# Optimization experiments

Measured on AMD Instinct MI355X. Metric: run time of the kernel, lower is better.

The kernel has to match this reference:

```python
import jax, jax.numpy as jnp
import numpy as np
import math

D_MODEL = 1024
HEADS = 16
HEAD_DIM = D_MODEL // HEADS
D_FF = 4096
EPS = 1e-5


def setup_inputs() -> dict:
    key = jax.random.key(0)
    ks = jax.random.split(key, 16)
    B, S, D = 4, 4096, D_MODEL
    s = 0.02
    return {
        "x": jax.random.normal(ks[0], (B, S, D), jnp.float32),
        "uncertainty": jax.random.uniform(ks[1], (HEADS,), jnp.float32),
        "Wq": jax.random.normal(ks[2], (D, D), jnp.float32) * s,
        "Wk": jax.random.normal(ks[3], (D, D), jnp.float32) * s,
        "Wv": jax.random.normal(ks[4], (D, D), jnp.float32) * s,
        "Wo": jax.random.normal(ks[5], (D, D), jnp.float32) * s,
        "bo": jnp.zeros((D,), jnp.float32),
        "ln1_g": jnp.ones((D,), jnp.float32),
        "ln1_b": jnp.zeros((D,), jnp.float32),
        "ln2_g": jnp.ones((D,), jnp.float32),
        "ln2_b": jnp.zeros((D,), jnp.float32),
        "W1": jax.random.normal(ks[6], (D, D_FF), jnp.float32) * s,
        "b1": jnp.zeros((D_FF,), jnp.float32),
        "W2": jax.random.normal(ks[7], (D_FF, D), jnp.float32) * s,
        "b2": jnp.zeros((D,), jnp.float32),
    }


def _layernorm(x, g, b):
    mu = jnp.mean(x, axis=-1, keepdims=True)
    var = jnp.mean(jnp.square(x - mu), axis=-1, keepdims=True)
    return (x - mu) * jax.lax.rsqrt(var + EPS) * g + b


def _attention(tmp, uncertainty, Wq, Wk, Wv, Wo, bo):
    B, S, D = tmp.shape
    # faithful to source: split_heads -> (B, S, head_dim, heads) via transpose(-2,-1)
    def split(y):
        return y.reshape(B, S, HEADS, HEAD_DIM).swapaxes(-2, -1)
    q = split(tmp @ Wq)  # (B,S,hd,H)
    k = split(tmp @ Wk)
    v = split(tmp @ Wv)
    scale = math.sqrt(HEAD_DIM) * jnp.sum(uncertainty)
    # per-token (head_dim x head_dim) scores, contracting over heads axis
    scores = jnp.einsum('bsih,bsjh->bsij', q, k) / scale  # (B,S,hd,hd)
    probs = jax.nn.softmax(scores, axis=-1)
    out = jnp.einsum('bsij,bsjh->bsih', probs, v)  # (B,S,hd,H)
    out = out.swapaxes(-2, -1).reshape(B, S, D)
    return out @ Wo + bo


def reference(x, uncertainty, Wq, Wk, Wv, Wo, bo, ln1_g, ln1_b, ln2_g, ln2_b, W1, b1, W2, b2):
    tmp = _layernorm(x, ln1_g, ln1_b)
    x = x + _attention(tmp, uncertainty, Wq, Wk, Wv, Wo, bo)  # dropout = identity (eval)
    tmp = _layernorm(x, ln2_g, ln2_b)
    ff = (jax.nn.gelu(tmp @ W1 + b1, approximate=False)) @ W2 + b2
    return x + ff
```

## Files before the change

kernel.cpp:

```cpp
#include <hip/hip_runtime.h>

typedef unsigned short u16;
typedef __attribute__((ext_vector_type(8))) short short8;
typedef __attribute__((ext_vector_type(4))) float f32x4;

static __device__ __forceinline__ float bf2f(u16 u) {
    union { unsigned int u; float f; } c; c.u = ((unsigned int)u) << 16; return c.f;
}
static __device__ __forceinline__ u16 f2bf(float f) {
    union { float f; unsigned int u; } c; c.f = f;
    unsigned int r = (c.u + 0x7fffu + ((c.u >> 16) & 1u)) >> 16;
    return (u16)r;
}

static __device__ __forceinline__ void glds16(const u16* g, u16* l) {
    __builtin_amdgcn_global_load_lds((const __attribute__((address_space(1))) unsigned int*)g,
                                     (__attribute__((address_space(3))) unsigned int*)l,
                                     16, 0, 0);
}

__global__ void wtrans_all(const float* __restrict__ q, const float* __restrict__ k,
                           const float* __restrict__ v, const float* __restrict__ o,
                           const float* __restrict__ w1, const float* __restrict__ w2,
                           u16* __restrict__ tqkv, u16* __restrict__ to_,
                           u16* __restrict__ t1, u16* __restrict__ t2) {
    const int id = blockIdx.x;
    const float* W; u16* D; int K, N, local;
    if (id < 3072) {
        const int which = id >> 10; local = id & 1023;
        W = which == 0 ? q : (which == 1 ? k : v);
        D = tqkv + (size_t)which * 1024 * 1024; K = 1024; N = 1024;
    } else if (id < 4096) { W = o;  D = to_; K = 1024; N = 1024; local = id - 3072; }
    else if (id < 8192)   { W = w1; D = t1;  K = 1024; N = 4096; local = id - 4096; }
    else                  { W = w2; D = t2;  K = 4096; N = 1024; local = id - 8192; }
    const int nx = N / 32;
    const int n0 = (local % nx) * 32, k0 = (local / nx) * 32;
    __shared__ float t[32][33];
    for (int i = threadIdx.y; i < 32; i += 8)
        t[i][threadIdx.x] = W[(size_t)(k0 + i) * N + n0 + threadIdx.x];
    __syncthreads();
    for (int i = threadIdx.y; i < 32; i += 8)
        D[(size_t)(n0 + i) * K + k0 + threadIdx.x] = f2bf(t[threadIdx.x][i]);
}

template <typename TI>
__global__ __launch_bounds__(256) void ln_kernel(const TI* __restrict__ x,
                                                 const float* __restrict__ g,
                                                 const float* __restrict__ b,
                                                 u16* __restrict__ out) {
    const int row = blockIdx.x;
    float4 v;
    if constexpr (sizeof(TI) == 4) {
        v = ((const float4*)((const float*)x + (size_t)row * 1024))[threadIdx.x];
    } else {
        ushort4 u = ((const ushort4*)((const u16*)x + (size_t)row * 1024))[threadIdx.x];
        v = make_float4(bf2f(u.x), bf2f(u.y), bf2f(u.z), bf2f(u.w));
    }
    float s = v.x + v.y + v.z + v.w;
    float ss = v.x * v.x + v.y * v.y + v.z * v.z + v.w * v.w;
    #pragma unroll
    for (int o = 32; o; o >>= 1) { s += __shfl_down(s, o); ss += __shfl_down(ss, o); }
    __shared__ float red[8];
    const int lane = threadIdx.x & 63, wave = threadIdx.x >> 6;
    if (lane == 0) { red[wave] = s; red[4 + wave] = ss; }
    __syncthreads();
    float S = red[0] + red[1] + red[2] + red[3];
    float SS = red[4] + red[5] + red[6] + red[7];
    float mu = S * (1.0f / 1024.0f);
    float var = SS * (1.0f / 1024.0f) - mu * mu;
    float rs = rsqrtf(var + 1e-5f);
    float4 gv = ((const float4*)g)[threadIdx.x];
    float4 bv = ((const float4*)b)[threadIdx.x];
    ushort4 o4;
    o4.x = f2bf((v.x - mu) * rs * gv.x + bv.x);
    o4.y = f2bf((v.y - mu) * rs * gv.y + bv.y);
    o4.z = f2bf((v.z - mu) * rs * gv.z + bv.z);
    o4.w = f2bf((v.w - mu) * rs * gv.w + bv.w);
    ((ushort4*)(out + (size_t)row * 1024))[threadIdx.x] = o4;
}

__global__ __launch_bounds__(256) void attn_kernel(const u16* __restrict__ QKV,
                                                   const float* __restrict__ unc,
                                                   u16* __restrict__ out) {
    __shared__ float kb[4][1024];
    __shared__ float vb[4][1024];
    const int tid = threadIdx.x;
    const int wave = tid >> 6, lane = tid & 63;
    const int tok = blockIdx.x * 4 + wave;
    const size_t baseq = (size_t)tok * 3072;

    #pragma unroll
    for (int e2 = 0; e2 < 2; e2++) {
        const int c = lane + 64 * e2;
        const int h = c >> 3, j0 = (c & 7) * 8;
        uint4 kraw = *(const uint4*)(QKV + baseq + 1024 + c * 8);
        uint4 vraw = *(const uint4*)(QKV + baseq + 2048 + c * 8);
        u16 kt[8], vt[8];
        *(uint4*)kt = kraw; *(uint4*)vt = vraw;
        #pragma unroll
        for (int e = 0; e < 8; e++) {
            kb[wave][(j0 + e) * 16 + h] = bf2f(kt[e]);
            vb[wave][(j0 + e) * 16 + h] = bf2f(vt[e]);
        }
    }
    float q[16];
    #pragma unroll
    for (int h = 0; h < 16; h++) q[h] = bf2f(QKV[baseq + h * 64 + lane]);
    float su = 0.0f;
    #pragma unroll
    for (int h = 0; h < 16; h++) su += unc[h];
    const float sinv = 1.0f / (8.0f * su);
    __syncthreads();

    float s[64];
    #pragma unroll
    for (int j = 0; j < 64; j++) {
        const float4* kr = (const float4*)&kb[wave][j * 16];
        float4 k0 = kr[0], k1 = kr[1], k2 = kr[2], k3 = kr[3];
        float a = q[0] * k0.x + q[1] * k0.y + q[2] * k0.z + q[3] * k0.w;
        a += q[4] * k1.x + q[5] * k1.y + q[6] * k1.z + q[7] * k1.w;
        a += q[8] * k2.x + q[9] * k2.y + q[10] * k2.z + q[11] * k2.w;
        a += q[12] * k3.x + q[13] * k3.y + q[14] * k3.z + q[15] * k3.w;
        s[j] = a;
    }
    float m = s[0];
    #pragma unroll
    for (int j = 1; j < 64; j++) m = fmaxf(m, s[j]);
    float sum = 0.0f;
    #pragma unroll
    for (int j = 0; j < 64; j++) { s[j] = __expf((s[j] - m) * sinv); sum += s[j]; }
    const float r = 1.0f / sum;
    float o[16];
    #pragma unroll
    for (int h = 0; h < 16; h++) o[h] = 0.0f;
    #pragma unroll
    for (int j = 0; j < 64; j++) {
        const float p = s[j];
        const float4* vr = (const float4*)&vb[wave][j * 16];
        float4 v0 = vr[0], v1 = vr[1], v2 = vr[2], v3 = vr[3];
        o[0] += p * v0.x; o[1] += p * v0.y; o[2] += p * v0.z; o[3] += p * v0.w;
        o[4] += p * v1.x; o[5] += p * v1.y; o[6] += p * v1.z; o[7] += p * v1.w;
        o[8] += p * v2.x; o[9] += p * v2.y; o[10] += p * v2.z; o[11] += p * v2.w;
        o[12] += p * v3.x; o[13] += p * v3.y; o[14] += p * v3.z; o[15] += p * v3.w;
    }
    const size_t baso = (size_t)tok * 1024;
    #pragma unroll
    for (int h = 0; h < 16; h++) out[baso + h * 64 + lane] = f2bf(o[h] * r);
}

template <int EPI>
__global__ __launch_bounds__(256, 2)
void gemm_kernel(const u16* __restrict__ A, const u16* __restrict__ Bt,
                 const float* __restrict__ bias, const void* __restrict__ res,
                 float* __restrict__ outF, u16* __restrict__ outB,
                 int N, int K) {
    __shared__ __align__(16) u16 As[128 * 64];
    __shared__ __align__(16) u16 Bs[128 * 64];
    const int tid = threadIdx.x;
    const int lane = tid & 63;
    const int wave = tid >> 6;
    const int wm = (wave >> 1) * 64;
    const int wn = (wave & 1) * 64;
    const int m0 = blockIdx.x * 128;
    const int n0 = blockIdx.y * 128;

    f32x4 acc[4][4];
    #pragma unroll
    for (int i = 0; i < 4; i++)
        #pragma unroll
        for (int j = 0; j < 4; j++) acc[i][j] = (f32x4){0.f, 0.f, 0.f, 0.f};

    const u16* aP[4];
    const u16* bP[4];
    #pragma unroll
    for (int e = 0; e < 4; e++) {
        const int c = tid + 256 * e;
        const int r = c >> 3;
        const int qg = (c & 7) ^ (r & 7);
        aP[e] = A + (size_t)(m0 + r) * K + qg * 8;
        bP[e] = Bt + (size_t)(n0 + r) * K + qg * 8;
    }

    for (int k0 = 0; k0 < K; k0 += 64) {
        __syncthreads();
        #pragma unroll
        for (int e = 0; e < 4; e++) {
            glds16(aP[e] + k0, &As[(tid + 256 * e) * 8]);
            glds16(bP[e] + k0, &Bs[(tid + 256 * e) * 8]);
        }
        __syncthreads();
        #pragma unroll
        for (int kk = 0; kk < 2; kk++) {
            const int Q = (lane >> 4) + kk * 4;
            short8 af[4], bf[4];
            #pragma unroll
            for (int i = 0; i < 4; i++) {
                const int R = wm + i * 16 + (lane & 15);
                af[i] = *(const short8*)&As[R * 64 + ((Q ^ (R & 7)) * 8)];
            }
            #pragma unroll
            for (int j = 0; j < 4; j++) {
                const int R = wn + j * 16 + (lane & 15);
                bf[j] = *(const short8*)&Bs[R * 64 + ((Q ^ (R & 7)) * 8)];
            }
            #pragma unroll
            for (int i = 0; i < 4; i++)
                #pragma unroll
                for (int j = 0; j < 4; j++)
                    acc[i][j] = __builtin_amdgcn_mfma_f32_16x16x32_bf16(af[i], bf[j], acc[i][j], 0, 0, 0);
        }
    }

    const int rbase = (lane >> 4) * 4;
    const int cidx = lane & 15;
    #pragma unroll
    for (int i = 0; i < 4; i++) {
        #pragma unroll
        for (int j = 0; j < 4; j++) {
            const int n = n0 + wn + j * 16 + cidx;
            #pragma unroll
            for (int r = 0; r < 4; r++) {
                const int m = m0 + wm + i * 16 + rbase + r;
                const size_t idx = (size_t)m * N + n;
                float v = acc[i][j][r];
                if (EPI == 0) {
                    outB[idx] = f2bf(v);
                } else if (EPI == 1) {
                    outF[idx] = v + bias[n] + bf2f(((const u16*)res)[idx]);
                } else if (EPI == 2) {
                    float t = v + bias[n];
                    t = 0.5f * t * (1.0f + erff(t * 0.70710678118654752f));
                    outB[idx] = f2bf(t);
                } else {
                    outB[idx] = f2bf(v + bias[n] + ((const float*)res)[idx]);
                }
            }
        }
    }
}

extern "C" void kernel_launch(void* const* d_in, const int* in_sizes, int n_in,
                              void* d_out, int out_size, void* d_ws, size_t ws_size,
                              hipStream_t stream) {
    const float* x    = (const float*)d_in[0];
    const float* unc  = (const float*)d_in[1];
    const float* Wq   = (const float*)d_in[2];
    const float* Wk   = (const float*)d_in[3];
    const float* Wv   = (const float*)d_in[4];
    const float* Wo   = (const float*)d_in[5];
    const float* bo   = (const float*)d_in[6];
    const float* ln1g = (const float*)d_in[7];
    const float* ln1b = (const float*)d_in[8];
    const float* ln2g = (const float*)d_in[9];
    const float* ln2b = (const float*)d_in[10];
    const float* W1   = (const float*)d_in[11];
    const float* b1   = (const float*)d_in[12];
    const float* W2   = (const float*)d_in[13];
    const float* b2   = (const float*)d_in[14];
    float* out = (float*)d_out;

    const int M = 16384;
    char* ws = (char*)d_ws;
    const size_t MB = 1024ull * 1024ull;
    u16* Wqkv = (u16*)(ws + 0 * MB);
    u16* Wto  = (u16*)(ws + 6 * MB);
    u16* Wt1  = (u16*)(ws + 8 * MB);
    u16* Wt2  = (u16*)(ws + 16 * MB);
    u16* Abuf = (u16*)(ws + 24 * MB);
    u16* QKVb = (u16*)(ws + 56 * MB);
    u16* Xr   = (u16*)(ws + 56 * MB);
    u16* FF1  = (u16*)(ws + 88 * MB);

    wtrans_all<<<12288, dim3(32, 8), 0, stream>>>(Wq, Wk, Wv, Wo, W1, W2,
                                                  Wqkv, Wto, Wt1, Wt2);

    ln_kernel<float><<<M, 256, 0, stream>>>(x, ln1g, ln1b, Abuf);

    gemm_kernel<0><<<dim3(128, 24), 256, 0, stream>>>(Abuf, Wqkv, nullptr, nullptr,
                                                      nullptr, QKVb, 3072, 1024);

    attn_kernel<<<M / 4, 256, 0, stream>>>(QKVb, unc, Abuf);

    gemm_kernel<3><<<dim3(128, 8), 256, 0, stream>>>(Abuf, Wto, bo, x, nullptr, Xr, 1024, 1024);

    ln_kernel<u16><<<M, 256, 0, stream>>>(Xr, ln2g, ln2b, Abuf);

    for (int c = 0; c < 2; c++) {
        const size_t ro = (size_t)c * 8192;
        gemm_kernel<2><<<dim3(64, 32), 256, 0, stream>>>(Abuf + ro * 1024, Wt1, b1, nullptr,
                                                         nullptr, FF1, 4096, 1024);
        gemm_kernel<1><<<dim3(64, 8), 256, 0, stream>>>(FF1, Wt2, b2, Xr + ro * 1024,
                                                        out + ro * 1024, nullptr, 1024, 4096);
    }
}
```

Measured before the change: 713.4 us.

## Replace 128x128 GEMM with double-buffered 256x256 8-wave pipelined GEMM

Replaces the single-buffered 128x128 GEMM with a 256x256 tile kernel using 512 threads. It double-buffers LDS and prefetches two K-steps ahead, interleaving half-tile loads with MFMA phases, raising wave priority during MFMA and swizzling the block order across XCDs. When workspace allows, it also runs the FFN GEMMs over all rows in one launch instead of two chunks. The change targets load latency, barrier stalls and launch count, at the cost of larger register and LDS use, which may reduce occupancy and increase tail effects on the smaller GEMMs.

```diff
diff --git a/kernel.cpp b/kernel.cpp
--- a/kernel.cpp
+++ b/kernel.cpp
@@ -149,88 +149,166 @@
 }
 
 template <int EPI>
-__global__ __launch_bounds__(256, 2)
-void gemm_kernel(const u16* __restrict__ A, const u16* __restrict__ Bt,
-                 const float* __restrict__ bias, const void* __restrict__ res,
-                 float* __restrict__ outF, u16* __restrict__ outB,
-                 int N, int K) {
-    __shared__ __align__(16) u16 As[128 * 64];
-    __shared__ __align__(16) u16 Bs[128 * 64];
+__global__ __launch_bounds__(512, 2)
+void gemm256_kernel(const u16* __restrict__ A, const u16* __restrict__ Bt,
+                    const float* __restrict__ bias, const void* __restrict__ res,
+                    float* __restrict__ outF, u16* __restrict__ outB,
+                    int N, int K, int gx) {
+    __shared__ __align__(16) u16 As[2][2][128 * 64];
+    __shared__ __align__(16) u16 Bs[2][2][128 * 64];
     const int tid = threadIdx.x;
     const int lane = tid & 63;
-    const int wave = tid >> 6;
-    const int wm = (wave >> 1) * 64;
-    const int wn = (wave & 1) * 64;
-    const int m0 = blockIdx.x * 128;
-    const int n0 = blockIdx.y * 128;
-
-    f32x4 acc[4][4];
-    #pragma unroll
-    for (int i = 0; i < 4; i++)
+    const int w = tid >> 6;
+    const int nwg = (int)gridDim.x;
+    const int lin = ((int)blockIdx.x & 7) * (nwg >> 3) + ((int)blockIdx.x >> 3);
+    const int m0 = (lin % gx) * 256;
+    const int n0 = (lin / gx) * 256;
+
+    f32x4 acc[8][4];
+    #pragma unroll
+    for (int i = 0; i < 8; i++)
         #pragma unroll
         for (int j = 0; j < 4; j++) acc[i][j] = (f32x4){0.f, 0.f, 0.f, 0.f};
 
-    const u16* aP[4];
-    const u16* bP[4];
-    #pragma unroll
-    for (int e = 0; e < 4; e++) {
-        const int c = tid + 256 * e;
+    const u16* aP[2][2];
+    const u16* bP[2][2];
+    int lo[2];
+    #pragma unroll
+    for (int e = 0; e < 2; e++) {
+        const int c = tid + 512 * e;
         const int r = c >> 3;
         const int qg = (c & 7) ^ (r & 7);
-        aP[e] = A + (size_t)(m0 + r) * K + qg * 8;
-        bP[e] = Bt + (size_t)(n0 + r) * K + qg * 8;
-    }
-
-    for (int k0 = 0; k0 < K; k0 += 64) {
-        __syncthreads();
-        #pragma unroll
-        for (int e = 0; e < 4; e++) {
-            glds16(aP[e] + k0, &As[(tid + 256 * e) * 8]);
-            glds16(bP[e] + k0, &Bs[(tid + 256 * e) * 8]);
-        }
-        __syncthreads();
-        #pragma unroll
-        for (int kk = 0; kk < 2; kk++) {
-            const int Q = (lane >> 4) + kk * 4;
-            short8 af[4], bf[4];
-            #pragma unroll
-            for (int i = 0; i < 4; i++) {
-                const int R = wm + i * 16 + (lane & 15);
-                af[i] = *(const short8*)&As[R * 64 + ((Q ^ (R & 7)) * 8)];
-            }
-            #pragma unroll
-            for (int j = 0; j < 4; j++) {
-                const int R = wn + j * 16 + (lane & 15);
-                bf[j] = *(const short8*)&Bs[R * 64 + ((Q ^ (R & 7)) * 8)];
-            }
-            #pragma unroll
-            for (int i = 0; i < 4; i++)
-                #pragma unroll
-                for (int j = 0; j < 4; j++)
-                    acc[i][j] = __builtin_amdgcn_mfma_f32_16x16x32_bf16(af[i], bf[j], acc[i][j], 0, 0, 0);
-        }
-    }
-
-    const int rbase = (lane >> 4) * 4;
-    const int cidx = lane & 15;
-    #pragma unroll
-    for (int i = 0; i < 4; i++) {
-        #pragma unroll
-        for (int j = 0; j < 4; j++) {
-            const int n = n0 + wn + j * 16 + cidx;
+        lo[e] = c * 8;
+        aP[e][0] = A + (size_t)(m0 + r) * K + qg * 8;
+        aP[e][1] = A + (size_t)(m0 + 128 + r) * K + qg * 8;
+        bP[e][0] = Bt + (size_t)(n0 + r) * K + qg * 8;
+        bP[e][1] = Bt + (size_t)(n0 + 128 + r) * K + qg * 8;
+    }
+    auto stgA = [&](int h, int t) {
+        glds16(aP[0][h] + t * 64, &As[t & 1][h][lo[0]]);
+        glds16(aP[1][h] + t * 64, &As[t & 1][h][lo[1]]);
+    };
+    auto stgB = [&](int h, int t) {
+        glds16(bP[0][h] + t * 64, &Bs[t & 1][h][lo[0]]);
+        glds16(bP[1][h] + t * 64, &Bs[t & 1][h][lo[1]]);
+    };
+
+    const int l15 = lane & 15;
+    const int sx0 = (((lane >> 4)) ^ (lane & 7)) * 8;
+    const int sx1 = (((lane >> 4) + 4) ^ (lane & 7)) * 8;
+    int rA[4], rB[2];
+    #pragma unroll
+    for (int i = 0; i < 4; i++) rA[i] = ((w >> 2) * 16 + i * 32 + l15) * 64;
+    #pragma unroll
+    for (int j = 0; j < 2; j++) rB[j] = ((w & 3) * 16 + j * 64 + l15) * 64;
+
+    const int NT = K >> 6;
+    stgA(0, 0); stgA(1, 0); stgB(0, 0); stgB(1, 0);
+    stgA(0, 1); stgA(1, 1); stgB(0, 1); stgB(1, 1);
+    asm volatile("s_waitcnt vmcnt(8)" ::: "memory");
+    __builtin_amdgcn_s_barrier();
+
+    for (int t = 0; t < NT; ++t) {
+        const int buf = t & 1;
+        short8 af[4][2], bf0[2][2], bf1[2][2];
+        #pragma unroll
+        for (int i = 0; i < 4; i++) {
+            af[i][0] = *(const short8*)&As[buf][0][rA[i] + sx0];
+            af[i][1] = *(const short8*)&As[buf][0][rA[i] + sx1];
+        }
+        #pragma unroll
+        for (int j = 0; j < 2; j++) {
+            bf0[j][0] = *(const short8*)&Bs[buf][0][rB[j] + sx0];
+            bf0[j][1] = *(const short8*)&Bs[buf][0][rB[j] + sx1];
+        }
+        __builtin_amdgcn_s_barrier();
+        asm volatile("s_waitcnt lgkmcnt(0)" ::: "memory");
+        __builtin_amdgcn_s_setprio(1);
+        #pragma unroll
+        for (int i = 0; i < 4; i++)
+            #pragma unroll
+            for (int j = 0; j < 2; j++) {
+                acc[i][j] = __builtin_amdgcn_mfma_f32_16x16x32_bf16(af[i][0], bf0[j][0], acc[i][j], 0, 0, 0);
+                acc[i][j] = __builtin_amdgcn_mfma_f32_16x16x32_bf16(af[i][1], bf0[j][1], acc[i][j], 0, 0, 0);
+            }
+        __builtin_amdgcn_s_setprio(0);
+        __builtin_amdgcn_s_barrier();
+
+        #pragma unroll
+        for (int j = 0; j < 2; j++) {
+            bf1[j][0] = *(const short8*)&Bs[buf][1][rB[j] + sx0];
+            bf1[j][1] = *(const short8*)&Bs[buf][1][rB[j] + sx1];
+        }
+        if (t + 2 < NT) { stgA(0, t + 2); stgB(0, t + 2); }
+        __builtin_amdgcn_s_barrier();
+        asm volatile("s_waitcnt lgkmcnt(0)" ::: "memory");
+        __builtin_amdgcn_s_setprio(1);
+        #pragma unroll
+        for (int i = 0; i < 4; i++)
+            #pragma unroll
+            for (int j = 0; j < 2; j++) {
+                acc[i][2 + j] = __builtin_amdgcn_mfma_f32_16x16x32_bf16(af[i][0], bf1[j][0], acc[i][2 + j], 0, 0, 0);
+                acc[i][2 + j] = __builtin_amdgcn_mfma_f32_16x16x32_bf16(af[i][1], bf1[j][1], acc[i][2 + j], 0, 0, 0);
+            }
+        __builtin_amdgcn_s_setprio(0);
+        __builtin_amdgcn_s_barrier();
+
+        #pragma unroll
+        for (int i = 0; i < 4; i++) {
+            af[i][0] = *(const short8*)&As[buf][1][rA[i] + sx0];
+            af[i][1] = *(const short8*)&As[buf][1][rA[i] + sx1];
+        }
+        if (t + 2 < NT) stgB(1, t + 2);
+        __builtin_amdgcn_s_barrier();
+        asm volatile("s_waitcnt lgkmcnt(0)" ::: "memory");
+        __builtin_amdgcn_s_setprio(1);
+        #pragma unroll
+        for (int i = 0; i < 4; i++)
+            #pragma unroll
+            for (int j = 0; j < 2; j++) {
+                acc[4 + i][2 + j] = __builtin_amdgcn_mfma_f32_16x16x32_bf16(af[i][0], bf1[j][0], acc[4 + i][2 + j], 0, 0, 0);
+                acc[4 + i][2 + j] = __builtin_amdgcn_mfma_f32_16x16x32_bf16(af[i][1], bf1[j][1], acc[4 + i][2 + j], 0, 0, 0);
+            }
+        __builtin_amdgcn_s_setprio(0);
+        __builtin_amdgcn_s_barrier();
+
+        if (t + 2 < NT) stgA(1, t + 2);
+        __builtin_amdgcn_s_setprio(1);
+        #pragma unroll
+        for (int i = 0; i < 4; i++)
+            #pragma unroll
+            for (int j = 0; j < 2; j++) {
+                acc[4 + i][j] = __builtin_amdgcn_mfma_f32_16x16x32_bf16(af[i][0], bf0[j][0], acc[4 + i][j], 0, 0, 0);
+                acc[4 + i][j] = __builtin_amdgcn_mfma_f32_16x16x32_bf16(af[i][1], bf0[j][1], acc[4 + i][j], 0, 0, 0);
+            }
+        __builtin_amdgcn_s_setprio(0);
+        if (t + 2 < NT) {
+            asm volatile("s_waitcnt vmcnt(8)" ::: "memory");
+        } else {
+            asm volatile("s_waitcnt vmcnt(0)" ::: "memory");
+        }
+        __builtin_amdgcn_s_barrier();
+    }
+
+    const int rb = (lane >> 4) * 4;
+    #pragma unroll
+    for (int I = 0; I < 8; I++) {
+        const int mB = m0 + (I >> 2) * 128 + (w >> 2) * 16 + (I & 3) * 32 + rb;
+        #pragma unroll
+        for (int J = 0; J < 4; J++) {
+            const int n = n0 + (J >> 1) * 128 + (w & 3) * 16 + (J & 1) * 64 + l15;
             #pragma unroll
             for (int r = 0; r < 4; r++) {
-                const int m = m0 + wm + i * 16 + rbase + r;
-                const size_t idx = (size_t)m * N + n;
-                float v = acc[i][j][r];
+                const size_t idx = (size_t)(mB + r) * N + n;
+                float v = acc[I][J][r];
                 if (EPI == 0) {
                     outB[idx] = f2bf(v);
                 } else if (EPI == 1) {
                     outF[idx] = v + bias[n] + bf2f(((const u16*)res)[idx]);
                 } else if (EPI == 2) {
-                    float t = v + bias[n];
-                    t = 0.5f * t * (1.0f + erff(t * 0.70710678118654752f));
-                    outB[idx] = f2bf(t);
+                    float tg = v + bias[n];
+                    tg = 0.5f * tg * (1.0f + erff(tg * 0.70710678118654752f));
+                    outB[idx] = f2bf(tg);
                 } else {
                     outB[idx] = f2bf(v + bias[n] + ((const float*)res)[idx]);
                 }
@@ -276,20 +354,27 @@
 
     ln_kernel<float><<<M, 256, 0, stream>>>(x, ln1g, ln1b, Abuf);
 
-    gemm_kernel<0><<<dim3(128, 24), 256, 0, stream>>>(Abuf, Wqkv, nullptr, nullptr,
-                                                      nullptr, QKVb, 3072, 1024);
+    gemm256_kernel<0><<<768, 512, 0, stream>>>(Abuf, Wqkv, nullptr, nullptr,
+                                               nullptr, QKVb, 3072, 1024, 64);
 
     attn_kernel<<<M / 4, 256, 0, stream>>>(QKVb, unc, Abuf);
 
-    gemm_kernel<3><<<dim3(128, 8), 256, 0, stream>>>(Abuf, Wto, bo, x, nullptr, Xr, 1024, 1024);
+    gemm256_kernel<3><<<256, 512, 0, stream>>>(Abuf, Wto, bo, x, nullptr, Xr, 1024, 1024, 64);
 
     ln_kernel<u16><<<M, 256, 0, stream>>>(Xr, ln2g, ln2b, Abuf);
 
-    for (int c = 0; c < 2; c++) {
-        const size_t ro = (size_t)c * 8192;
-        gemm_kernel<2><<<dim3(64, 32), 256, 0, stream>>>(Abuf + ro * 1024, Wt1, b1, nullptr,
-                                                         nullptr, FF1, 4096, 1024);
-        gemm_kernel<1><<<dim3(64, 8), 256, 0, stream>>>(FF1, Wt2, b2, Xr + ro * 1024,
-                                                        out + ro * 1024, nullptr, 1024, 4096);
-    }
-}
+    if (ws_size >= 216ull * MB) {
+        gemm256_kernel<2><<<1024, 512, 0, stream>>>(Abuf, Wt1, b1, nullptr,
+                                                    nullptr, FF1, 4096, 1024, 64);
+        gemm256_kernel<1><<<256, 512, 0, stream>>>(FF1, Wt2, b2, Xr,
+                                                   out, nullptr, 1024, 4096, 64);
+    } else {
+        for (int c = 0; c < 2; c++) {
+            const size_t ro = (size_t)c * 8192;
+            gemm256_kernel<2><<<512, 512, 0, stream>>>(Abuf + ro * 1024, Wt1, b1, nullptr,
+                                                       nullptr, FF1, 4096, 1024, 32);
+            gemm256_kernel<1><<<128, 512, 0, stream>>>(FF1, Wt2, b2, Xr + ro * 1024,
+                                                       out + ro * 1024, nullptr, 1024, 4096, 32);
+        }
+    }
+}
```

Result: slower. 778.4 us (+9.1%).
